# Kernel tuning notes

Hardware: AMD Instinct MI355X
Metric: run time of the kernel (lower is better)

## Reference

```python
import jax, jax.numpy as jnp
import numpy as np

IMG_CENTER = 112.0  # init arg; normalize() is unused in forward
EPS = 1e-12


def setup_inputs() -> dict:
    key = jax.random.key(0)
    kp, kg, km = jax.random.split(key, 3)
    B, N, M = 8, 4096, 4096
    pred = jax.random.normal(kp, (B, N, 3), jnp.float32)
    gt = jax.random.normal(kg, (B, M, 3), jnp.float32)
    # near-identity extrinsics with z-translation 5 so the perspective divide is stable
    base = jnp.concatenate([jnp.eye(3, dtype=jnp.float32),
                            jnp.array([[0.0], [0.0], [5.0]], jnp.float32)], axis=1)  # [3,4]
    proMatrix = base[None, :, :] + 0.05 * jax.random.normal(km, (B, 3, 4), jnp.float32)
    return {"pred": pred, "gt": gt, "proMatrix": proMatrix}


def _project(x, P):
    # x: [B, n, 3], P: [B, 3, 4] -> [B, n, 2] image-plane coords
    B, n, _ = x.shape
    hom = jnp.concatenate([x, jnp.ones((B, n, 1), x.dtype)], axis=2)  # [B, n, 4]
    posed = jnp.einsum('bij,bnj->bni', P, hom)                         # [B, n, 3]
    return posed[..., :2] / posed[..., 2:3]


def _chamfer(a, b):
    # a: [B, N, 2], b: [B, M, 2]; L2-norm (not squared) bidirectional chamfer
    d2 = (jnp.sum(a * a, -1)[:, :, None]
          + jnp.sum(b * b, -1)[:, None, :]
          - 2.0 * jnp.einsum('bnd,bmd->bnm', a, b))  # [B, N, M]
    d = jnp.sqrt(jnp.maximum(d2, EPS))
    per_b = jnp.mean(jnp.min(d, axis=2), axis=1) + jnp.mean(jnp.min(d, axis=1), axis=1)
    return jnp.mean(per_b)


def reference(pred, gt, proMatrix):
    gt_plane = _project(gt, proMatrix)
    pred_plane = _project(pred, proMatrix)
    return _chamfer(gt_plane, pred_plane)
```

## Files before the change

kernel.cpp:

```cpp
#include <hip/hip_runtime.h>
#include <math.h>

#define NPTS 4096
#define NB 8
#define NQTOT (2*NB*NPTS)
#define EPSF 1e-12f
#define NCHUNK 16
#define CCH 256
#define QPT 4
#define RBLK 64

typedef float f32x2 __attribute__((ext_vector_type(2)));

static __device__ __forceinline__ f32x2 pk_fma_bx(f32x2 a, f32x2 b, f32x2 c){
    f32x2 d;
    asm("v_pk_fma_f32 %0, %1, %2, %3 op_sel:[0,0,0] op_sel_hi:[1,0,0]"
        : "=v"(d) : "v"(a), "v"(b), "v"(c));
    return d;
}
static __device__ __forceinline__ f32x2 pk_fma_by(f32x2 a, f32x2 b, f32x2 c){
    f32x2 d;
    asm("v_pk_fma_f32 %0, %1, %2, %3 op_sel:[0,1,0] op_sel_hi:[1,1,1]"
        : "=v"(d) : "v"(a), "v"(b), "v"(c));
    return d;
}
static __device__ __forceinline__ float fmin3(float a, float b, float c){
    float d;
    asm("v_min3_f32 %0, %1, %2, %3" : "=v"(d) : "v"(a), "v"(b), "v"(c));
    return d;
}

static __device__ __forceinline__ void project_pt(const float* __restrict__ p3,
                                                  const float* __restrict__ Pb,
                                                  float& ix, float& iy){
    float x = p3[0], y = p3[1], z = p3[2];
    float px = fmaf(Pb[0],x, fmaf(Pb[1],y, fmaf(Pb[2],z,  Pb[3])));
    float py = fmaf(Pb[4],x, fmaf(Pb[5],y, fmaf(Pb[6],z,  Pb[7])));
    float pz = fmaf(Pb[8],x, fmaf(Pb[9],y, fmaf(Pb[10],z, Pb[11])));
    ix = px / pz;
    iy = py / pz;
}

__global__ __launch_bounds__(256) void chamfer_fused(
        const float* __restrict__ pred, const float* __restrict__ gt,
        const float* __restrict__ P, float* __restrict__ minpart,
        unsigned* __restrict__ counter){
    __shared__ float4 cand[CCH];
    int bid   = blockIdx.x;
    int chunk = bid & 15;
    int qq    = (bid >> 4) & 3;
    int b     = (bid >> 6) & 7;
    int dir   = (bid >> 9) & 1;
    int t = threadIdx.x;

    if (bid == 0 && t == 0) *counter = 0;

    const float* Pb   = P + b * 12;
    const float* qsrc = dir ? pred : gt;
    const float* csrc = dir ? gt : pred;

    {
        const float* p3 = csrc + (size_t)(b*NPTS + chunk*CCH + t) * 3;
        float cx, cy; project_pt(p3, Pb, cx, cy);
        cand[t] = make_float4(-2.0f*cx, -2.0f*cy, fmaf(cx,cx, cy*cy), 0.0f);
    }

    f32x2 axp[QPT/2], ayp[QPT/2];
    float a2[QPT];
    #pragma unroll
    for (int q = 0; q < QPT; ++q){
        int qi = qq*1024 + q*256 + t;
        const float* p3 = qsrc + (size_t)(b*NPTS + qi) * 3;
        float ix, iy; project_pt(p3, Pb, ix, iy);
        axp[q>>1][q&1] = ix;
        ayp[q>>1][q&1] = iy;
        a2[q] = fmaf(ix,ix, iy*iy);
    }
    float mn[QPT];
    #pragma unroll
    for (int q = 0; q < QPT; ++q) mn[q] = 3.4e38f;

    __syncthreads();

    #pragma unroll 4
    for (int ci = 0; ci < CCH; ci += 2){
        float4 cd0 = cand[ci];
        float4 cd1 = cand[ci+1];
        f32x2 c0lo = {cd0.x, cd0.y}, c0hi = {cd0.z, cd0.w};
        f32x2 c1lo = {cd1.x, cd1.y}, c1hi = {cd1.z, cd1.w};
        #pragma unroll
        for (int p = 0; p < QPT/2; ++p){
            f32x2 t0 = pk_fma_bx(axp[p], c0lo, c0hi);
            t0 = pk_fma_by(ayp[p], c0lo, t0);
            f32x2 t1 = pk_fma_bx(axp[p], c1lo, c1hi);
            t1 = pk_fma_by(ayp[p], c1lo, t1);
            mn[2*p]   = fmin3(t0.x, t1.x, mn[2*p]);
            mn[2*p+1] = fmin3(t0.y, t1.y, mn[2*p+1]);
        }
    }

    int gq = dir*(NB*NPTS) + b*NPTS + qq*1024 + t;
    #pragma unroll
    for (int q = 0; q < QPT; ++q){
        minpart[(size_t)chunk*NQTOT + gq + q*256] = mn[q] + a2[q];
    }
}

__global__ __launch_bounds__(1024) void reduce_all(
        const float* __restrict__ minpart, float* __restrict__ partials,
        unsigned* __restrict__ counter, float* __restrict__ out){
    __shared__ float sm[1024];
    __shared__ int last;
    int t = threadIdx.x;
    int i = blockIdx.x * 1024 + t;
    float m0 = minpart[i];
    #pragma unroll
    for (int c = 1; c < NCHUNK; ++c) m0 = fminf(m0, minpart[(size_t)c*NQTOT + i]);
    sm[t] = sqrtf(fmaxf(m0, EPSF));
    __syncthreads();
    #pragma unroll
    for (int o = 512; o > 0; o >>= 1){
        if (t < o) sm[t] += sm[t + o];
        __syncthreads();
    }
    if (t == 0){
        __hip_atomic_store(&partials[blockIdx.x], sm[0],
                           __ATOMIC_RELEASE, __HIP_MEMORY_SCOPE_AGENT);
        unsigned prev = __hip_atomic_fetch_add(counter, 1u,
                           __ATOMIC_ACQ_REL, __HIP_MEMORY_SCOPE_AGENT);
        last = (prev == RBLK - 1);
    }
    __syncthreads();
    if (!last) return;

    if (t < RBLK){
        sm[t] = __hip_atomic_load(&partials[t],
                    __ATOMIC_ACQUIRE, __HIP_MEMORY_SCOPE_AGENT);
    }
    __syncthreads();
    #pragma unroll
    for (int o = RBLK/2; o > 0; o >>= 1){
        if (t < o) sm[t] += sm[t + o];
        __syncthreads();
    }
    if (t == 0) out[0] = sm[0] * (1.0f / 32768.0f);
}

extern "C" void kernel_launch(void* const* d_in, const int* in_sizes, int n_in,
                              void* d_out, int out_size, void* d_ws, size_t ws_size,
                              hipStream_t stream) {
    const float* pred = (const float*)d_in[0];
    const float* gt   = (const float*)d_in[1];
    const float* P    = (const float*)d_in[2];
    float* out = (float*)d_out;

    const size_t MINPART_BYTES = (size_t)NCHUNK * NQTOT * 4;
    float*    minpart  = (float*)d_ws;
    float*    partials = (float*)((char*)d_ws + MINPART_BYTES);
    unsigned* counter  = (unsigned*)((char*)d_ws + MINPART_BYTES + 4096);

    chamfer_fused<<<1024, 256, 0, stream>>>(pred, gt, P, minpart, counter);
    reduce_all<<<RBLK, 1024, 0, stream>>>(minpart, partials, counter, out);
}
```

Baseline: 28.56 us.

## Double queries per thread, split candidate LDS layout, reshape reduce grid

Each thread now handles eight query points instead of four, which halves the chamfer grid to 512 blocks and amortizes every candidate LDS read over more FMAs. Candidates are stored as a packed xy float2 array plus a separate squared-norm array, so four candidates come in with three 16-byte loads instead of four. New op_sel variants select which norm lane feeds the packed FMA. The reduction now runs 256 blocks of 256 threads rather than 64 of 1024. The costs are higher register pressure and fewer blocks to spread across the GPU's compute units.

```diff
diff --git a/kernel.cpp b/kernel.cpp
--- a/kernel.cpp
+++ b/kernel.cpp
@@ -7,14 +7,20 @@
 #define EPSF 1e-12f
 #define NCHUNK 16
 #define CCH 256
-#define QPT 4
-#define RBLK 64
+#define QPT 8
+#define RBLK 256
 
 typedef float f32x2 __attribute__((ext_vector_type(2)));
 
-static __device__ __forceinline__ f32x2 pk_fma_bx(f32x2 a, f32x2 b, f32x2 c){
+static __device__ __forceinline__ f32x2 pk_fma_bx_c0(f32x2 a, f32x2 b, f32x2 c){
     f32x2 d;
     asm("v_pk_fma_f32 %0, %1, %2, %3 op_sel:[0,0,0] op_sel_hi:[1,0,0]"
+        : "=v"(d) : "v"(a), "v"(b), "v"(c));
+    return d;
+}
+static __device__ __forceinline__ f32x2 pk_fma_bx_c1(f32x2 a, f32x2 b, f32x2 c){
+    f32x2 d;
+    asm("v_pk_fma_f32 %0, %1, %2, %3 op_sel:[0,0,1] op_sel_hi:[1,0,1]"
         : "=v"(d) : "v"(a), "v"(b), "v"(c));
     return d;
 }
@@ -45,12 +51,13 @@
         const float* __restrict__ pred, const float* __restrict__ gt,
         const float* __restrict__ P, float* __restrict__ minpart,
         unsigned* __restrict__ counter){
-    __shared__ float4 cand[CCH];
+    __shared__ __align__(16) float2 sxy[CCH];
+    __shared__ __align__(16) float  sz [CCH];
     int bid   = blockIdx.x;
     int chunk = bid & 15;
-    int qq    = (bid >> 4) & 3;
-    int b     = (bid >> 6) & 7;
-    int dir   = (bid >> 9) & 1;
+    int qhalf = (bid >> 4) & 1;
+    int b     = (bid >> 5) & 7;
+    int dir   = (bid >> 8) & 1;
     int t = threadIdx.x;
 
     if (bid == 0 && t == 0) *counter = 0;
@@ -62,14 +69,15 @@
     {
         const float* p3 = csrc + (size_t)(b*NPTS + chunk*CCH + t) * 3;
         float cx, cy; project_pt(p3, Pb, cx, cy);
-        cand[t] = make_float4(-2.0f*cx, -2.0f*cy, fmaf(cx,cx, cy*cy), 0.0f);
+        sxy[t] = make_float2(-2.0f*cx, -2.0f*cy);
+        sz[t]  = fmaf(cx,cx, cy*cy);
     }
 
     f32x2 axp[QPT/2], ayp[QPT/2];
     float a2[QPT];
     #pragma unroll
     for (int q = 0; q < QPT; ++q){
-        int qi = qq*1024 + q*256 + t;
+        int qi = qhalf*2048 + q*256 + t;
         const float* p3 = qsrc + (size_t)(b*NPTS + qi) * 3;
         float ix, iy; project_pt(p3, Pb, ix, iy);
         axp[q>>1][q&1] = ix;
@@ -82,44 +90,51 @@
 
     __syncthreads();
 
-    #pragma unroll 4
-    for (int ci = 0; ci < CCH; ci += 2){
-        float4 cd0 = cand[ci];
-        float4 cd1 = cand[ci+1];
-        f32x2 c0lo = {cd0.x, cd0.y}, c0hi = {cd0.z, cd0.w};
-        f32x2 c1lo = {cd1.x, cd1.y}, c1hi = {cd1.z, cd1.w};
+    const float4* sxy4 = (const float4*)sxy;
+    const float4* sz4  = (const float4*)sz;
+
+    #pragma unroll 2
+    for (int c4 = 0; c4 < CCH/4; ++c4){
+        float4 xy01 = sxy4[2*c4];
+        float4 xy23 = sxy4[2*c4 + 1];
+        float4 zq   = sz4[c4];
+        f32x2 b0 = {xy01.x, xy01.y}, b1 = {xy01.z, xy01.w};
+        f32x2 b2 = {xy23.x, xy23.y}, b3 = {xy23.z, xy23.w};
+        f32x2 z01 = {zq.x, zq.y},   z23 = {zq.z, zq.w};
         #pragma unroll
         for (int p = 0; p < QPT/2; ++p){
-            f32x2 t0 = pk_fma_bx(axp[p], c0lo, c0hi);
-            t0 = pk_fma_by(ayp[p], c0lo, t0);
-            f32x2 t1 = pk_fma_bx(axp[p], c1lo, c1hi);
-            t1 = pk_fma_by(ayp[p], c1lo, t1);
+            f32x2 t0 = pk_fma_by(ayp[p], b0, pk_fma_bx_c0(axp[p], b0, z01));
+            f32x2 t1 = pk_fma_by(ayp[p], b1, pk_fma_bx_c1(axp[p], b1, z01));
+            f32x2 t2 = pk_fma_by(ayp[p], b2, pk_fma_bx_c0(axp[p], b2, z23));
+            f32x2 t3 = pk_fma_by(ayp[p], b3, pk_fma_bx_c1(axp[p], b3, z23));
             mn[2*p]   = fmin3(t0.x, t1.x, mn[2*p]);
+            mn[2*p]   = fmin3(t2.x, t3.x, mn[2*p]);
             mn[2*p+1] = fmin3(t0.y, t1.y, mn[2*p+1]);
+            mn[2*p+1] = fmin3(t2.y, t3.y, mn[2*p+1]);
         }
     }
 
-    int gq = dir*(NB*NPTS) + b*NPTS + qq*1024 + t;
+    int gq = dir*(NB*NPTS) + b*NPTS + qhalf*2048 + t;
     #pragma unroll
     for (int q = 0; q < QPT; ++q){
         minpart[(size_t)chunk*NQTOT + gq + q*256] = mn[q] + a2[q];
     }
 }
 
-__global__ __launch_bounds__(1024) void reduce_all(
+__global__ __launch_bounds__(256) void reduce_all(
         const float* __restrict__ minpart, float* __restrict__ partials,
         unsigned* __restrict__ counter, float* __restrict__ out){
-    __shared__ float sm[1024];
+    __shared__ float sm[256];
     __shared__ int last;
     int t = threadIdx.x;
-    int i = blockIdx.x * 1024 + t;
+    int i = blockIdx.x * 256 + t;
     float m0 = minpart[i];
     #pragma unroll
     for (int c = 1; c < NCHUNK; ++c) m0 = fminf(m0, minpart[(size_t)c*NQTOT + i]);
     sm[t] = sqrtf(fmaxf(m0, EPSF));
     __syncthreads();
     #pragma unroll
-    for (int o = 512; o > 0; o >>= 1){
+    for (int o = 128; o > 0; o >>= 1){
         if (t < o) sm[t] += sm[t + o];
         __syncthreads();
     }
@@ -133,13 +148,11 @@
     __syncthreads();
     if (!last) return;
 
-    if (t < RBLK){
-        sm[t] = __hip_atomic_load(&partials[t],
-                    __ATOMIC_ACQUIRE, __HIP_MEMORY_SCOPE_AGENT);
-    }
+    sm[t] = __hip_atomic_load(&partials[t],
+                __ATOMIC_ACQUIRE, __HIP_MEMORY_SCOPE_AGENT);
     __syncthreads();
     #pragma unroll
-    for (int o = RBLK/2; o > 0; o >>= 1){
+    for (int o = 128; o > 0; o >>= 1){
         if (t < o) sm[t] += sm[t + o];
         __syncthreads();
     }
@@ -159,6 +172,6 @@
     float*    partials = (float*)((char*)d_ws + MINPART_BYTES);
     unsigned* counter  = (unsigned*)((char*)d_ws + MINPART_BYTES + 4096);
 
-    chamfer_fused<<<1024, 256, 0, stream>>>(pred, gt, P, minpart, counter);
-    reduce_all<<<RBLK, 1024, 0, stream>>>(minpart, partials, counter, out);
+    chamfer_fused<<<512, 256, 0, stream>>>(pred, gt, P, minpart, counter);
+    reduce_all<<<RBLK, 256, 0, stream>>>(minpart, partials, counter, out);
 }
```

Result: slower. 32.77 us (+14.7%).
